# Optimization experiments

Hardware: AMD Instinct MI355X
Metric: run time of the kernel (lower is better)

The kernel has to match this reference:

```python
import jax, jax.numpy as jnp
import numpy as np

N_CAMS = 6
Y, X, Z = 8, 256, 256      # voxel grid (height, x, z)
H, W = 224, 400            # image size used by project_world2img scale
XV, ZV = 56, 100           # img_feats spatial dims [BS,C,XV,ZV]
EPS = 1e-6


def setup_inputs():
    key = jax.random.key(0)
    k1, k2, k3 = jax.random.split(key, 3)
    BS, C = N_CAMS, 32
    img_feats = jax.random.normal(k1, (BS, C, XV, ZV), jnp.float32)
    variances = jax.random.uniform(k2, (BS, 1, H, W), jnp.float32)
    render_depth = jax.random.uniform(k3, (BS, 1, H, W), jnp.float32) * 50.0
    # voxel sample coords, ordering matches crop_base: (x_patch, z_patch, height)
    hs = jnp.linspace(-1.0, 3.0, Y)
    xs = jnp.linspace(-24.0, 24.0, X)
    zs = jnp.linspace(-24.0, 24.0, Z)
    hh, px, pz = jnp.meshgrid(hs, xs, zs, indexing='ij')
    sample_coords = jnp.stack([px, pz, hh], -1).reshape(1, Y * X * Z, 3)
    # six surround cameras at origin, yaw-rotated, looking horizontally (cam2world)
    Ps = np.zeros((N_CAMS, 4, 4), np.float32)
    for i in range(N_CAMS):
        a = i * (2.0 * np.pi / N_CAMS)
        c, s = np.cos(a), np.sin(a)
        # columns are camera x/y/z axes in world coords (y down, z forward)
        Ps[i, :3, :3] = np.array([[s, 0.0, c], [-c, 0.0, s], [0.0, -1.0, 0.0]], np.float32)
        Ps[i, 3, 3] = 1.0
    Ks = np.tile(np.array([[250.0, 0.0, W / 2.0], [0.0, 250.0, H / 2.0], [0.0, 0.0, 1.0]],
                          np.float32), (N_CAMS, 1, 1))
    return {"img_feats": img_feats, "variances": variances, "render_depth": render_depth,
            "sample_coords": sample_coords, "Ps": jnp.asarray(Ps), "Ks": jnp.asarray(Ks)}


def _grid_sample_2d(feat, gx, gy):
    # feat [BS,C,Hf,Wf]; gx,gy [BS,N] normalized to [-1,1].
    # torch.grid_sample bilinear, padding_mode='zeros', align_corners=False
    BS, C, Hf, Wf = feat.shape
    x = (gx + 1.0) * (Wf * 0.5) - 0.5
    y = (gy + 1.0) * (Hf * 0.5) - 0.5
    x0 = jnp.floor(x)
    y0 = jnp.floor(y)
    wx, wy = x - x0, y - y0
    flat = feat.reshape(BS, C, Hf * Wf)
    out = jnp.zeros((BS, C, gx.shape[1]), feat.dtype)
    for dx, dy, wgt in ((0, 0, (1 - wx) * (1 - wy)), (1, 0, wx * (1 - wy)),
                        (0, 1, (1 - wx) * wy), (1, 1, wx * wy)):
        xi = x0 + dx
        yi = y0 + dy
        valid = (xi >= 0) & (xi < Wf) & (yi >= 0) & (yi < Hf)
        idx = (jnp.clip(yi, 0, Hf - 1) * Wf + jnp.clip(xi, 0, Wf - 1)).astype(jnp.int32)
        v = jnp.take_along_axis(flat, idx[:, None, :], axis=2)  # [BS,C,N]
        out = out + v * (wgt * valid)[:, None, :]
    return out


def _masked_mean(x, m, axis):
    # reduce_masked_mean: sum(x*m)/ (sum(m)+eps) along axis
    return jnp.sum(x * m, axis=axis) / (jnp.sum(m, axis=axis) + EPS)


def reference(img_feats, variances, render_depth, sample_coords, Ps, Ks):
    BS, C = img_feats.shape[:2]
    B = BS // N_CAMS
    N = sample_coords.shape[1]
    # --- project_world2img: world -> cam -> pixel ---
    pts_h = jnp.concatenate([sample_coords, jnp.ones((1, N, 1), sample_coords.dtype)], -1)
    w2c = jnp.linalg.inv(Ps)                                    # [BS,4,4]
    cam = jnp.einsum('bij,anj->bni', w2c[:, :3, :], pts_h)      # [BS,N,3]
    uvw = jnp.einsum('bij,bnj->bni', Ks, cam)                   # [BS,N,3]
    zc = uvw[..., 2]
    zsafe = jnp.where(jnp.abs(zc) < 1e-6, 1e-6, zc)
    u = uvw[..., 0] / zsafe
    v = uvw[..., 1] / zsafe
    pix = jnp.nan_to_num(jnp.stack([v, u], -1), nan=-1.0)       # (row, col), scale (H, W)
    mask = (zc > 1e-3) & (u >= 0) & (u < W) & (v >= 0) & (v < H)
    # samp_ind = pix / [H, W] * 2 - 1; coord0 indexes width of permuted feat
    gx = pix[..., 0] / H * 2.0 - 1.0
    gy = pix[..., 1] / W * 2.0 - 1.0
    mf = mask.reshape(B, N_CAMS, 1, Y, X, Z).astype(img_feats.dtype)
    # feature lift: grid_sample on img_feats.permute(0,1,3,2) -> [BS,C,ZV,XV]
    out = _grid_sample_2d(jnp.swapaxes(img_feats, 2, 3), gx, gy)
    out = out.reshape(B, N_CAMS, C, Y, X, Z)
    out_feats = _masked_mean(out, mf, 1).reshape(B, C * Y, X, Z)
    # variance info branch
    var = _grid_sample_2d(jnp.swapaxes(variances, 2, 3), gx, gy)
    var_info = _masked_mean(var.reshape(B, N_CAMS, 1, Y, X, Z), mf, 1).reshape(B, Y, X, Z)
    # depth info branch
    nd = _grid_sample_2d(jnp.swapaxes(render_depth, 2, 3), gx, gy)
    nerf_depth = _masked_mean(nd.reshape(B, N_CAMS, 1, Y, X, Z), mf, 1)  # [B,1,Y,X,Z]
    depth = _masked_mean(zc.reshape(B, N_CAMS, 1, Y, X, Z), mf, 1)       # [B,1,Y,X,Z]
    return (out_feats, var_info, depth, nerf_depth)
```

## Files before the change

kernel.cpp:

```cpp
#include <hip/hip_runtime.h>
#include <math.h>

#define NCAMS 6
#define CCH   32
#define YY    8
#define XX    256
#define ZZ    256
#define NVOX  (YY*XX*ZZ)
#define IMG_H 224
#define IMG_W 400
#define FXV   56
#define FZV   100

#define NF (NCAMS*FXV*FZV)
#define NV (NCAMS*IMG_H*IMG_W)
#define FEATS_T_ELEMS (NF*CCH)
#define VD_T_ELEMS    (NV*2)
#define WS_NEED_BYTES ((size_t)(FEATS_T_ELEMS + VD_T_ELEMS) * 4)

__global__ __launch_bounds__(256) void prep_all(
    const float* __restrict__ src_f, const float* __restrict__ var,
    const float* __restrict__ dep, float* __restrict__ dst_f,
    float* __restrict__ dst_vd)
{
    int t = blockIdx.x * 256 + threadIdx.x;
    if (t < NF) {
        int b = t / (FXV * FZV);
        int r = t - b * (FXV * FZV);
        float4* d4 = (float4*)(dst_f + (size_t)t * CCH);
        #pragma unroll
        for (int j = 0; j < CCH / 4; j++) {
            float4 v;
            v.x = src_f[(size_t)(b * CCH + 4*j + 0) * (FXV*FZV) + r];
            v.y = src_f[(size_t)(b * CCH + 4*j + 1) * (FXV*FZV) + r];
            v.z = src_f[(size_t)(b * CCH + 4*j + 2) * (FXV*FZV) + r];
            v.w = src_f[(size_t)(b * CCH + 4*j + 3) * (FXV*FZV) + r];
            d4[j] = v;
        }
    } else {
        int u = t - NF;
        if (u < NV) ((float2*)dst_vd)[u] = make_float2(var[u], dep[u]);
    }
}

__global__ __launch_bounds__(64) void mvmap_fast(
    const float* __restrict__ feats_t,
    const float* __restrict__ vd_t,
    const float* __restrict__ coords,
    const float* __restrict__ Ps,
    const float* __restrict__ Ks,
    float* __restrict__ out)
{
    __shared__ float4 sW2C[NCAMS][3];
    __shared__ float4 sK[NCAMS][3];
    __shared__ float  sT[64 * 33];

    int lane = threadIdx.x;
    if (lane < NCAMS) {
        int b = lane;
        const float* P = Ps + b * 16;
        float r00=P[0], r01=P[1], r02=P[2],  tx=P[3];
        float r10=P[4], r11=P[5], r12=P[6],  ty=P[7];
        float r20=P[8], r21=P[9], r22=P[10], tz=P[11];
        float det = r00*(r11*r22 - r12*r21)
                  - r01*(r10*r22 - r12*r20)
                  + r02*(r10*r21 - r11*r20);
        float id = 1.0f / det;
        float i00 =  (r11*r22 - r12*r21) * id;
        float i01 = -(r01*r22 - r02*r21) * id;
        float i02 =  (r01*r12 - r02*r11) * id;
        float i10 = -(r10*r22 - r12*r20) * id;
        float i11 =  (r00*r22 - r02*r20) * id;
        float i12 = -(r00*r12 - r02*r10) * id;
        float i20 =  (r10*r21 - r11*r20) * id;
        float i21 = -(r00*r21 - r01*r20) * id;
        float i22 =  (r00*r11 - r01*r10) * id;
        sW2C[b][0] = make_float4(i00, i01, i02, -(i00*tx + i01*ty + i02*tz));
        sW2C[b][1] = make_float4(i10, i11, i12, -(i10*tx + i11*ty + i12*tz));
        sW2C[b][2] = make_float4(i20, i21, i22, -(i20*tx + i21*ty + i22*tz));
        sK[b][0] = make_float4(Ks[b*9+0], Ks[b*9+1], Ks[b*9+2], 0.f);
        sK[b][1] = make_float4(Ks[b*9+3], Ks[b*9+4], Ks[b*9+5], 0.f);
        sK[b][2] = make_float4(Ks[b*9+6], Ks[b*9+7], Ks[b*9+8], 0.f);
    }
    __syncthreads();

    int n0 = blockIdx.x * 64;
    int n  = n0 + lane;

    float px = coords[3*n + 0];
    float pz = coords[3*n + 1];
    float ph = coords[3*n + 2];

    float wsum = 0.0f, zsum = 0.0f;
    int   nvis = 0;
    float s_u[3] = {0.f, 0.f, 0.f};
    float s_v[3] = {0.f, 0.f, 0.f};
    int   s_b[3] = {0, 0, 0};

    #pragma unroll
    for (int b = 0; b < NCAMS; b++) {
        float4 r0 = sW2C[b][0], r1 = sW2C[b][1], r2 = sW2C[b][2];
        float cx = r0.x*px + r0.y*pz + r0.z*ph + r0.w;
        float cy = r1.x*px + r1.y*pz + r1.z*ph + r1.w;
        float cz = r2.x*px + r2.y*pz + r2.z*ph + r2.w;
        float4 k0 = sK[b][0], k1 = sK[b][1], k2 = sK[b][2];
        float u0 = k0.x*cx + k0.y*cy + k0.z*cz;
        float v0 = k1.x*cx + k1.y*cy + k1.z*cz;
        float zc = k2.x*cx + k2.y*cy + k2.z*cz;
        float zsafe = (fabsf(zc) < 1e-6f) ? 1e-6f : zc;
        float u = u0 / zsafe;
        float v = v0 / zsafe;
        bool mask = (zc > 1e-3f) && (u >= 0.0f) && (u < (float)IMG_W)
                                 && (v >= 0.0f) && (v < (float)IMG_H);
        wsum += mask ? 1.0f : 0.0f;
        zsum += mask ? zc : 0.0f;
        bool c0 = mask && (nvis == 0);
        bool c1 = mask && (nvis == 1);
        bool c2 = mask && (nvis == 2);
        s_u[0] = c0 ? u : s_u[0];  s_v[0] = c0 ? v : s_v[0];  s_b[0] = c0 ? b : s_b[0];
        s_u[1] = c1 ? u : s_u[1];  s_v[1] = c1 ? v : s_v[1];  s_b[1] = c1 ? b : s_b[1];
        s_u[2] = c2 ? u : s_u[2];  s_v[2] = c2 ? v : s_v[2];  s_b[2] = c2 ? b : s_b[2];
        nvis += mask ? 1 : 0;
    }
    float invd = 1.0f / (wsum + 1e-6f);

    float vsum = 0.0f, ndsum = 0.0f;
    #pragma unroll
    for (int it = 0; it < 3; it++) {
        if (it < nvis) {
            float u = s_u[it], v = s_v[it];
            int   b = s_b[it];
            float xf = v - 0.5f;
            float yf = u - 0.5f;
            float x0f = floorf(xf), y0f = floorf(yf);
            float wx = xf - x0f, wy = yf - y0f;
            int x0 = (int)x0f, y0 = (int)y0f;
            float vx0 = (x0   >= 0 && x0   < IMG_H) ? 1.0f : 0.0f;
            float vx1 = (x0+1 >= 0 && x0+1 < IMG_H) ? 1.0f : 0.0f;
            float vy0 = (y0   >= 0 && y0   < IMG_W) ? 1.0f : 0.0f;
            float vy1 = (y0+1 >= 0 && y0+1 < IMG_W) ? 1.0f : 0.0f;
            float w00 = (1.0f-wx)*(1.0f-wy)*vx0*vy0;
            float w10 = wx*(1.0f-wy)*vx1*vy0;
            float w01 = (1.0f-wx)*wy*vx0*vy1;
            float w11 = wx*wy*vx1*vy1;
            int xi0 = min(max(x0,   0), IMG_H-1), xi1 = min(max(x0+1, 0), IMG_H-1);
            int yi0 = min(max(y0,   0), IMG_W-1), yi1 = min(max(y0+1, 0), IMG_W-1);
            const float2* pv = (const float2*)(vd_t) + (size_t)b * (IMG_H*IMG_W);
            float2 t00 = pv[xi0*IMG_W + yi0], t01 = pv[xi0*IMG_W + yi1];
            float2 t10 = pv[xi1*IMG_W + yi0], t11 = pv[xi1*IMG_W + yi1];
            vsum  += w00*t00.x + w01*t01.x + w10*t10.x + w11*t11.x;
            ndsum += w00*t00.y + w01*t01.y + w10*t10.y + w11*t11.y;
        }
    }
    __builtin_nontemporal_store(vsum  * invd, &out[(size_t)CCH*NVOX + n]);
    __builtin_nontemporal_store(zsum  * invd, &out[(size_t)CCH*NVOX + NVOX + n]);
    __builtin_nontemporal_store(ndsum * invd, &out[(size_t)CCH*NVOX + 2*(size_t)NVOX + n]);

    int cg = lane & 7;
    int vg = lane >> 3;

    #pragma unroll
    for (int s = 0; s < 8; s++) {
        int src = 8*s + vg;

        int   nv  = __shfl(nvis, src);
        float iv  = __shfl(invd, src);
        float uu0 = __shfl(s_u[0], src), vv0 = __shfl(s_v[0], src);
        float uu1 = __shfl(s_u[1], src), vv1 = __shfl(s_v[1], src);
        float uu2 = __shfl(s_u[2], src), vv2 = __shfl(s_v[2], src);
        int   bb0 = __shfl(s_b[0], src);
        int   bb1 = __shfl(s_b[1], src);
        int   bb2 = __shfl(s_b[2], src);
        float uu[3] = {uu0, uu1, uu2};
        float vv[3] = {vv0, vv1, vv2};
        int   bb[3] = {bb0, bb1, bb2};

        float ax = 0.f, ay = 0.f, az = 0.f, aw = 0.f;
        #pragma unroll
        for (int it = 0; it < 3; it++) {
            if (it < nv) {
                float u = uu[it], v = vv[it];
                int   b = bb[it];
                float xf = v * 0.25f - 0.5f;
                float yf = u * 0.25f - 0.5f;
                float x0f = floorf(xf), y0f = floorf(yf);
                float wx = xf - x0f, wy = yf - y0f;
                int x0 = (int)x0f, y0 = (int)y0f;
                float vx0 = (x0   >= 0 && x0   < FXV) ? 1.0f : 0.0f;
                float vx1 = (x0+1 >= 0 && x0+1 < FXV) ? 1.0f : 0.0f;
                float vy0 = (y0   >= 0 && y0   < FZV) ? 1.0f : 0.0f;
                float vy1 = (y0+1 >= 0 && y0+1 < FZV) ? 1.0f : 0.0f;
                float w00 = (1.0f-wx)*(1.0f-wy)*vx0*vy0;
                float w10 = wx*(1.0f-wy)*vx1*vy0;
                float w01 = (1.0f-wx)*wy*vx0*vy1;
                float w11 = wx*wy*vx1*vy1;
                int xi0 = min(max(x0,   0), FXV-1), xi1 = min(max(x0+1, 0), FXV-1);
                int yi0 = min(max(y0,   0), FZV-1), yi1 = min(max(y0+1, 0), FZV-1);
                const float* base = feats_t + (size_t)b * (FXV*FZV*CCH) + cg * 4;
                float4 a  = *(const float4*)(base + (size_t)(xi0*FZV + yi0)*CCH);
                float4 b2 = *(const float4*)(base + (size_t)(xi0*FZV + yi1)*CCH);
                float4 c2 = *(const float4*)(base + (size_t)(xi1*FZV + yi0)*CCH);
                float4 d2 = *(const float4*)(base + (size_t)(xi1*FZV + yi1)*CCH);
                ax += w00*a.x + w01*b2.x + w10*c2.x + w11*d2.x;
                ay += w00*a.y + w01*b2.y + w10*c2.y + w11*d2.y;
                az += w00*a.z + w01*b2.z + w10*c2.z + w11*d2.z;
                aw += w00*a.w + w01*b2.w + w10*c2.w + w11*d2.w;
            }
        }
        float* p = &sT[(8*s + vg) * 33 + cg * 4];
        p[0] = ax * iv;
        p[1] = ay * iv;
        p[2] = az * iv;
        p[3] = aw * iv;
    }
    __syncthreads();

    #pragma unroll
    for (int c = 0; c < CCH; c++) {
        float val = sT[lane * 33 + c];
        __builtin_nontemporal_store(val, &out[(size_t)c * NVOX + n]);
    }
}

__global__ __launch_bounds__(256) void mvmap_main(
    const float* __restrict__ img_feats,
    const float* __restrict__ variances,
    const float* __restrict__ render_depth,
    const float* __restrict__ coords,
    const float* __restrict__ Ps,
    const float* __restrict__ Ks,
    float* __restrict__ out)
{
    __shared__ float sW2C[NCAMS][12];
    __shared__ float sK[NCAMS][9];

    if (threadIdx.x < NCAMS) {
        int b = threadIdx.x;
        const float* P = Ps + b * 16;
        float r00=P[0], r01=P[1], r02=P[2],  tx=P[3];
        float r10=P[4], r11=P[5], r12=P[6],  ty=P[7];
        float r20=P[8], r21=P[9], r22=P[10], tz=P[11];
        float det = r00*(r11*r22 - r12*r21)
                  - r01*(r10*r22 - r12*r20)
                  + r02*(r10*r21 - r11*r20);
        float id = 1.0f / det;
        float i00 =  (r11*r22 - r12*r21) * id;
        float i01 = -(r01*r22 - r02*r21) * id;
        float i02 =  (r01*r12 - r02*r11) * id;
        float i10 = -(r10*r22 - r12*r20) * id;
        float i11 =  (r00*r22 - r02*r20) * id;
        float i12 = -(r00*r12 - r02*r10) * id;
        float i20 =  (r10*r21 - r11*r20) * id;
        float i21 = -(r00*r21 - r01*r20) * id;
        float i22 =  (r00*r11 - r01*r10) * id;
        sW2C[b][0]=i00; sW2C[b][1]=i01; sW2C[b][2] =i02; sW2C[b][3] =-(i00*tx + i01*ty + i02*tz);
        sW2C[b][4]=i10; sW2C[b][5]=i11; sW2C[b][6] =i12; sW2C[b][7] =-(i10*tx + i11*ty + i12*tz);
        sW2C[b][8]=i20; sW2C[b][9]=i21; sW2C[b][10]=i22; sW2C[b][11]=-(i20*tx + i21*ty + i22*tz);
        #pragma unroll
        for (int jj = 0; jj < 9; jj++) sK[b][jj] = Ks[b*9 + jj];
    }
    __syncthreads();

    int n = blockIdx.x * blockDim.x + threadIdx.x;
    if (n >= NVOX) return;

    float px = coords[3*n + 0];
    float pz = coords[3*n + 1];
    float ph = coords[3*n + 2];

    float fsum[CCH];
    #pragma unroll
    for (int c = 0; c < CCH; c++) fsum[c] = 0.0f;
    float wsum = 0.0f, vsum = 0.0f, ndsum = 0.0f, zsum = 0.0f;

    for (int b = 0; b < NCAMS; b++) {
        float cx = sW2C[b][0]*px + sW2C[b][1]*pz + sW2C[b][2] *ph + sW2C[b][3];
        float cy = sW2C[b][4]*px + sW2C[b][5]*pz + sW2C[b][6] *ph + sW2C[b][7];
        float cz = sW2C[b][8]*px + sW2C[b][9]*pz + sW2C[b][10]*ph + sW2C[b][11];
        float u0 = sK[b][0]*cx + sK[b][1]*cy + sK[b][2]*cz;
        float v0 = sK[b][3]*cx + sK[b][4]*cy + sK[b][5]*cz;
        float zc = sK[b][6]*cx + sK[b][7]*cy + sK[b][8]*cz;
        float zsafe = (fabsf(zc) < 1e-6f) ? 1e-6f : zc;
        float u = u0 / zsafe;
        float v = v0 / zsafe;
        bool mask = (zc > 1e-3f) && (u >= 0.0f) && (u < (float)IMG_W)
                                 && (v >= 0.0f) && (v < (float)IMG_H);
        if (!mask) continue;

        wsum += 1.0f;
        zsum += zc;
        {
            float xf = v * 0.25f - 0.5f;
            float yf = u * 0.25f - 0.5f;
            float x0f = floorf(xf), y0f = floorf(yf);
            float wx = xf - x0f, wy = yf - y0f;
            int x0 = (int)x0f, y0 = (int)y0f;
            float vx0 = (x0   >= 0 && x0   < FXV) ? 1.0f : 0.0f;
            float vx1 = (x0+1 >= 0 && x0+1 < FXV) ? 1.0f : 0.0f;
            float vy0 = (y0   >= 0 && y0   < FZV) ? 1.0f : 0.0f;
            float vy1 = (y0+1 >= 0 && y0+1 < FZV) ? 1.0f : 0.0f;
            float w00 = (1.0f-wx)*(1.0f-wy)*vx0*vy0;
            float w10 = wx*(1.0f-wy)*vx1*vy0;
            float w01 = (1.0f-wx)*wy*vx0*vy1;
            float w11 = wx*wy*vx1*vy1;
            int xi0 = min(max(x0,   0), FXV-1), xi1 = min(max(x0+1, 0), FXV-1);
            int yi0 = min(max(y0,   0), FZV-1), yi1 = min(max(y0+1, 0), FZV-1);
            int o00 = xi0*FZV + yi0, o01 = xi0*FZV + yi1;
            int o10 = xi1*FZV + yi0, o11 = xi1*FZV + yi1;
            const float* p = img_feats + (size_t)b * (CCH*FXV*FZV);
            #pragma unroll
            for (int c = 0; c < CCH; c++) {
                const float* pc = p + c * (FXV*FZV);
                fsum[c] += w00*pc[o00] + w01*pc[o01] + w10*pc[o10] + w11*pc[o11];
            }
        }
        {
            float xf = v - 0.5f;
            float yf = u - 0.5f;
            float x0f = floorf(xf), y0f = floorf(yf);
            float wx = xf - x0f, wy = yf - y0f;
            int x0 = (int)x0f, y0 = (int)y0f;
            float vx0 = (x0   >= 0 && x0   < IMG_H) ? 1.0f : 0.0f;
            float vx1 = (x0+1 >= 0 && x0+1 < IMG_H) ? 1.0f : 0.0f;
            float vy0 = (y0   >= 0 && y0   < IMG_W) ? 1.0f : 0.0f;
            float vy1 = (y0+1 >= 0 && y0+1 < IMG_W) ? 1.0f : 0.0f;
            float w00 = (1.0f-wx)*(1.0f-wy)*vx0*vy0;
            float w10 = wx*(1.0f-wy)*vx1*vy0;
            float w01 = (1.0f-wx)*wy*vx0*vy1;
            float w11 = wx*wy*vx1*vy1;
            int xi0 = min(max(x0,   0), IMG_H-1), xi1 = min(max(x0+1, 0), IMG_H-1);
            int yi0 = min(max(y0,   0), IMG_W-1), yi1 = min(max(y0+1, 0), IMG_W-1);
            int o00 = xi0*IMG_W + yi0, o01 = xi0*IMG_W + yi1;
            int o10 = xi1*IMG_W + yi0, o11 = xi1*IMG_W + yi1;
            const float* pv = variances    + (size_t)b * (IMG_H*IMG_W);
            const float* pd = render_depth + (size_t)b * (IMG_H*IMG_W);
            vsum  += w00*pv[o00] + w01*pv[o01] + w10*pv[o10] + w11*pv[o11];
            ndsum += w00*pd[o00] + w01*pd[o01] + w10*pd[o10] + w11*pd[o11];
        }
    }

    float invd = 1.0f / (wsum + 1e-6f);
    #pragma unroll
    for (int c = 0; c < CCH; c++) out[(size_t)c * NVOX + n] = fsum[c] * invd;
    out[(size_t)CCH*NVOX + n]              = vsum  * invd;
    out[(size_t)CCH*NVOX + NVOX + n]       = zsum  * invd;
    out[(size_t)CCH*NVOX + 2*(size_t)NVOX + n] = ndsum * invd;
}

extern "C" void kernel_launch(void* const* d_in, const int* in_sizes, int n_in,
                              void* d_out, int out_size, void* d_ws, size_t ws_size,
                              hipStream_t stream) {
    const float* img_feats    = (const float*)d_in[0];
    const float* variances    = (const float*)d_in[1];
    const float* render_depth = (const float*)d_in[2];
    const float* coords       = (const float*)d_in[3];
    const float* Ps           = (const float*)d_in[4];
    const float* Ks           = (const float*)d_in[5];
    float* out = (float*)d_out;

    if (ws_size >= WS_NEED_BYTES) {
        float* feats_t = (float*)d_ws;
        float* vd_t    = feats_t + FEATS_T_ELEMS;
        {
            int total = NF + NV;
            hipLaunchKernelGGL(prep_all, dim3((total + 255) / 256), dim3(256), 0, stream,
                               img_feats, variances, render_depth, feats_t, vd_t);
        }
        hipLaunchKernelGGL(mvmap_fast, dim3(NVOX / 64), dim3(64), 0, stream,
                           feats_t, vd_t, coords, Ps, Ks, out);
    } else {
        hipLaunchKernelGGL(mvmap_main, dim3(NVOX / 256), dim3(256), 0, stream,
                           img_feats, variances, render_depth, coords, Ps, Ks, out);
    }
}
```

Baseline: 41.14 us.

## Use 256-thread blocks with per-wave half-tile LDS transpose in mvmap_fast

Moves mvmap_fast from 64-thread blocks to 256-thread blocks of four wavefronts, with a launch-bounds occupancy hint. Each wave now stages its 64 voxels in two passes of 32 rows, so the LDS transpose buffer per wave shrinks to half. Each output store then writes 32 consecutive voxels for two channels. The aim is to cut shared memory per voxel, lift occupancy and reduce per-block setup overhead. The cost is two extra block-wide barriers per pass and shorter contiguous store runs per channel.

```diff
diff --git a/kernel.cpp b/kernel.cpp
--- a/kernel.cpp
+++ b/kernel.cpp
@@ -43,7 +43,7 @@
     }
 }
 
-__global__ __launch_bounds__(64) void mvmap_fast(
+__global__ __launch_bounds__(256, 8) void mvmap_fast(
     const float* __restrict__ feats_t,
     const float* __restrict__ vd_t,
     const float* __restrict__ coords,
@@ -53,11 +53,10 @@
 {
     __shared__ float4 sW2C[NCAMS][3];
     __shared__ float4 sK[NCAMS][3];
-    __shared__ float  sT[64 * 33];
-
-    int lane = threadIdx.x;
-    if (lane < NCAMS) {
-        int b = lane;
+    __shared__ float  sT[4][32 * 33];
+
+    if (threadIdx.x < NCAMS) {
+        int b = threadIdx.x;
         const float* P = Ps + b * 16;
         float r00=P[0], r01=P[1], r02=P[2],  tx=P[3];
         float r10=P[4], r11=P[5], r12=P[6],  ty=P[7];
@@ -84,8 +83,10 @@
     }
     __syncthreads();
 
-    int n0 = blockIdx.x * 64;
-    int n  = n0 + lane;
+    int wv   = threadIdx.x >> 6;
+    int lane = threadIdx.x & 63;
+    int n0   = blockIdx.x * 256 + wv * 64;
+    int n    = n0 + lane;
 
     float px = coords[3*n + 0];
     float pz = coords[3*n + 1];
@@ -160,65 +161,74 @@
     int vg = lane >> 3;
 
     #pragma unroll
-    for (int s = 0; s < 8; s++) {
-        int src = 8*s + vg;
-
-        int   nv  = __shfl(nvis, src);
-        float iv  = __shfl(invd, src);
-        float uu0 = __shfl(s_u[0], src), vv0 = __shfl(s_v[0], src);
-        float uu1 = __shfl(s_u[1], src), vv1 = __shfl(s_v[1], src);
-        float uu2 = __shfl(s_u[2], src), vv2 = __shfl(s_v[2], src);
-        int   bb0 = __shfl(s_b[0], src);
-        int   bb1 = __shfl(s_b[1], src);
-        int   bb2 = __shfl(s_b[2], src);
-        float uu[3] = {uu0, uu1, uu2};
-        float vv[3] = {vv0, vv1, vv2};
-        int   bb[3] = {bb0, bb1, bb2};
-
-        float ax = 0.f, ay = 0.f, az = 0.f, aw = 0.f;
+    for (int p = 0; p < 2; p++) {
         #pragma unroll
-        for (int it = 0; it < 3; it++) {
-            if (it < nv) {
-                float u = uu[it], v = vv[it];
-                int   b = bb[it];
-                float xf = v * 0.25f - 0.5f;
-                float yf = u * 0.25f - 0.5f;
-                float x0f = floorf(xf), y0f = floorf(yf);
-                float wx = xf - x0f, wy = yf - y0f;
-                int x0 = (int)x0f, y0 = (int)y0f;
-                float vx0 = (x0   >= 0 && x0   < FXV) ? 1.0f : 0.0f;
-                float vx1 = (x0+1 >= 0 && x0+1 < FXV) ? 1.0f : 0.0f;
-                float vy0 = (y0   >= 0 && y0   < FZV) ? 1.0f : 0.0f;
-                float vy1 = (y0+1 >= 0 && y0+1 < FZV) ? 1.0f : 0.0f;
-                float w00 = (1.0f-wx)*(1.0f-wy)*vx0*vy0;
-                float w10 = wx*(1.0f-wy)*vx1*vy0;
-                float w01 = (1.0f-wx)*wy*vx0*vy1;
-                float w11 = wx*wy*vx1*vy1;
-                int xi0 = min(max(x0,   0), FXV-1), xi1 = min(max(x0+1, 0), FXV-1);
-                int yi0 = min(max(y0,   0), FZV-1), yi1 = min(max(y0+1, 0), FZV-1);
-                const float* base = feats_t + (size_t)b * (FXV*FZV*CCH) + cg * 4;
-                float4 a  = *(const float4*)(base + (size_t)(xi0*FZV + yi0)*CCH);
-                float4 b2 = *(const float4*)(base + (size_t)(xi0*FZV + yi1)*CCH);
-                float4 c2 = *(const float4*)(base + (size_t)(xi1*FZV + yi0)*CCH);
-                float4 d2 = *(const float4*)(base + (size_t)(xi1*FZV + yi1)*CCH);
-                ax += w00*a.x + w01*b2.x + w10*c2.x + w11*d2.x;
-                ay += w00*a.y + w01*b2.y + w10*c2.y + w11*d2.y;
-                az += w00*a.z + w01*b2.z + w10*c2.z + w11*d2.z;
-                aw += w00*a.w + w01*b2.w + w10*c2.w + w11*d2.w;
+        for (int sr = 0; sr < 4; sr++) {
+            int s   = 4*p + sr;
+            int src = 8*s + vg;
+
+            int   nv  = __shfl(nvis, src);
+            float iv  = __shfl(invd, src);
+            float uu0 = __shfl(s_u[0], src), vv0 = __shfl(s_v[0], src);
+            float uu1 = __shfl(s_u[1], src), vv1 = __shfl(s_v[1], src);
+            float uu2 = __shfl(s_u[2], src), vv2 = __shfl(s_v[2], src);
+            int   bb0 = __shfl(s_b[0], src);
+            int   bb1 = __shfl(s_b[1], src);
+            int   bb2 = __shfl(s_b[2], src);
+            float uu[3] = {uu0, uu1, uu2};
+            float vv[3] = {vv0, vv1, vv2};
+            int   bb[3] = {bb0, bb1, bb2};
+
+            float ax = 0.f, ay = 0.f, az = 0.f, aw = 0.f;
+            #pragma unroll
+            for (int it = 0; it < 3; it++) {
+                if (it < nv) {
+                    float u = uu[it], v = vv[it];
+                    int   b = bb[it];
+                    float xf = v * 0.25f - 0.5f;
+                    float yf = u * 0.25f - 0.5f;
+                    float x0f = floorf(xf), y0f = floorf(yf);
+                    float wx = xf - x0f, wy = yf - y0f;
+                    int x0 = (int)x0f, y0 = (int)y0f;
+                    float vx0 = (x0   >= 0 && x0   < FXV) ? 1.0f : 0.0f;
+                    float vx1 = (x0+1 >= 0 && x0+1 < FXV) ? 1.0f : 0.0f;
+                    float vy0 = (y0   >= 0 && y0   < FZV) ? 1.0f : 0.0f;
+                    float vy1 = (y0+1 >= 0 && y0+1 < FZV) ? 1.0f : 0.0f;
+                    float w00 = (1.0f-wx)*(1.0f-wy)*vx0*vy0;
+                    float w10 = wx*(1.0f-wy)*vx1*vy0;
+                    float w01 = (1.0f-wx)*wy*vx0*vy1;
+                    float w11 = wx*wy*vx1*vy1;
+                    int xi0 = min(max(x0,   0), FXV-1), xi1 = min(max(x0+1, 0), FXV-1);
+                    int yi0 = min(max(y0,   0), FZV-1), yi1 = min(max(y0+1, 0), FZV-1);
+                    const float* base = feats_t + (size_t)b * (FXV*FZV*CCH) + cg * 4;
+                    float4 a  = *(const float4*)(base + (size_t)(xi0*FZV + yi0)*CCH);
+                    float4 b2 = *(const float4*)(base + (size_t)(xi0*FZV + yi1)*CCH);
+                    float4 c2 = *(const float4*)(base + (size_t)(xi1*FZV + yi0)*CCH);
+                    float4 d2 = *(const float4*)(base + (size_t)(xi1*FZV + yi1)*CCH);
+                    ax += w00*a.x + w01*b2.x + w10*c2.x + w11*d2.x;
+                    ay += w00*a.y + w01*b2.y + w10*c2.y + w11*d2.y;
+                    az += w00*a.z + w01*b2.z + w10*c2.z + w11*d2.z;
+                    aw += w00*a.w + w01*b2.w + w10*c2.w + w11*d2.w;
+                }
             }
-        }
-        float* p = &sT[(8*s + vg) * 33 + cg * 4];
-        p[0] = ax * iv;
-        p[1] = ay * iv;
-        p[2] = az * iv;
-        p[3] = aw * iv;
-    }
-    __syncthreads();
-
-    #pragma unroll
-    for (int c = 0; c < CCH; c++) {
-        float val = sT[lane * 33 + c];
-        __builtin_nontemporal_store(val, &out[(size_t)c * NVOX + n]);
+            float* pt = &sT[wv][(8*sr + vg) * 33 + cg * 4];
+            pt[0] = ax * iv;
+            pt[1] = ay * iv;
+            pt[2] = az * iv;
+            pt[3] = aw * iv;
+        }
+        __syncthreads();
+
+        int row  = lane & 31;
+        int half = lane >> 5;
+        int vn   = n0 + 32*p + row;
+        #pragma unroll
+        for (int i = 0; i < 16; i++) {
+            int c = 2*i + half;
+            float val = sT[wv][row * 33 + c];
+            __builtin_nontemporal_store(val, &out[(size_t)c * NVOX + vn]);
+        }
+        __syncthreads();
     }
 }
 
@@ -366,7 +376,7 @@
             hipLaunchKernelGGL(prep_all, dim3((total + 255) / 256), dim3(256), 0, stream,
                                img_feats, variances, render_depth, feats_t, vd_t);
         }
-        hipLaunchKernelGGL(mvmap_fast, dim3(NVOX / 64), dim3(64), 0, stream,
+        hipLaunchKernelGGL(mvmap_fast, dim3(NVOX / 256), dim3(256), 0, stream,
                            feats_t, vd_t, coords, Ps, Ks, out);
     } else {
         hipLaunchKernelGGL(mvmap_main, dim3(NVOX / 256), dim3(256), 0, stream,
```

New measurement: 47.65 us. 1.16x slower.
